# Optimization experiments

Measured on AMD Instinct MI355X. Metric: run time of the kernel, lower is better.

The kernel has to match this reference:

```python
import jax, jax.numpy as jnp
import numpy as np

N = 8192          # num atoms
APM = 32          # atoms per molecule
M = N // APM      # 256 molecules
FEAT = 100        # hidden_channels == num_filters
NG = 25           # num gaussians
K = 28            # knn neighbors
L = 4             # num interaction blocks
CUTOFF = 6.0
LOG2 = float(np.log(2.0))


def ssp(x):
    # pyg ShiftedSoftplus: softplus(x) - log(2)
    return jax.nn.softplus(x) - LOG2


def setup_inputs() -> dict:
    key = jax.random.key(0)
    ks = jax.random.split(key, 16)
    z = jax.random.randint(ks[0], (N,), 1, 100)
    pos = jax.random.normal(ks[1], (N, 3), jnp.float32) * 2.0
    ptr = jnp.arange(0, N + APM, APM)  # [M+1] molecule boundaries

    def w(k, shape, fan):
        return (jax.random.normal(k, shape, jnp.float32) / np.sqrt(fan)).astype(jnp.float32)

    def b(k, shape):
        return jax.random.normal(k, shape, jnp.float32) * 0.01

    kb = jax.random.split(ks[15], 8)
    H = FEAT // 2
    return {
        "z": z,
        "pos": pos,
        "ptr": ptr,
        "emb": jax.random.normal(ks[2], (100, FEAT), jnp.float32),
        "mlp_w1": w(ks[3], (L, NG, FEAT), NG),
        "mlp_b1": b(kb[0], (L, FEAT)),
        "mlp_w2": w(ks[4], (L, FEAT, FEAT), FEAT),
        "mlp_b2": b(kb[1], (L, FEAT)),
        "lin1_w": w(ks[5], (L, FEAT, FEAT), FEAT),
        "lin2_w": w(ks[6], (L, FEAT, FEAT), FEAT),
        "lin2_b": b(kb[2], (L, FEAT)),
        "lin_w": w(ks[7], (L, FEAT, FEAT), FEAT),
        "lin_b": b(kb[3], (L, FEAT)),
        "out_w1": w(ks[8], (FEAT, H), FEAT),
        "out_b1": b(kb[4], (H,)),
        "out_w2": w(ks[9], (H, 1), H),
        "out_b2": b(kb[5], (1,)),
    }


def reference(z, pos, ptr, emb, mlp_w1, mlp_b1, mlp_w2, mlp_b2,
              lin1_w, lin2_w, lin2_b, lin_w, lin_b,
              out_w1, out_b1, out_w2, out_b2):
    n = z.shape[0]
    m = ptr.shape[0] - 1

    # ptr -> per-atom batch ids (index_fill + cumsum; OOB index N dropped)
    flag = jnp.zeros((n,), jnp.int32).at[ptr].set(1, mode="drop")
    flag = flag.at[0].set(0)
    batch = jnp.cumsum(flag)

    # ---- KNN interaction graph (full NxN pairwise distances + masking + topk)
    diff = pos[:, None, :] - pos[None, :, :]           # [N,N,3]
    d2 = jnp.sum(diff * diff, axis=-1)                  # [N,N]
    ar = jnp.arange(n)
    mask = (ar[:, None] == ar[None, :]) \
         | (batch[:, None] != batch[None, :]) \
         | (d2 > CUTOFF * CUTOFF)
    dist = jnp.where(mask, CUTOFF, jnp.sqrt(jnp.where(mask, 1.0, d2)))
    neg, idx = jax.lax.top_k(-dist, K)                  # k nearest per row
    ew = -neg.reshape(-1)                               # edge distances [N*K]
    src = idx.reshape(-1)                               # source atoms j; target of edge (i,m) is i

    # ---- Gaussian smearing
    offset = jnp.linspace(0.0, CUTOFF, NG)
    coeff = -0.5 / (offset[1] - offset[0]) ** 2
    ea = jnp.exp(coeff * (ew[:, None] - offset[None, :]) ** 2)  # [E,NG]

    # cosine cutoff (zero weight for padded edges at dist==cutoff)
    ccut = 0.5 * (jnp.cos(ew * jnp.pi / CUTOFF) + 1.0)          # [E]

    h = emb[z]                                                   # [N,F]
    f = h.shape[1]
    for l in range(L):
        # filter network on edge attributes
        Wf = ssp(ea @ mlp_w1[l] + mlp_b1[l]) @ mlp_w2[l] + mlp_b2[l]
        Wf = Wf * ccut[:, None]                                  # [E,F]
        # CFConv: lin1 -> gather*filter -> sum over k neighbors -> lin2
        x1 = h @ lin1_w[l]                                       # [N,F]
        msg = x1[src] * Wf                                       # [E,F]
        agg = msg.reshape(n, K, f).sum(axis=1)                   # each node i has exactly K incoming edges
        v = ssp(agg @ lin2_w[l] + lin2_b[l]) @ lin_w[l] + lin_b[l]
        h = h + v

    # readout head
    h = ssp(h @ out_w1 + out_b1)
    per_atom = (h @ out_w2 + out_b2).reshape(-1)                 # [N]
    return jax.ops.segment_sum(per_atom, batch, num_segments=m) # per-molecule energy [M]
```

## Files before the change

### kernel.cpp

```cpp
#include <hip/hip_runtime.h>
#include <math.h>

#define APM   32
#define NMOL  256
#define FEAT  100
#define NPAD  112
#define LAYERS 4
#define NTHREADS 1024
#define NWAVES   16
#define G_TBL 1024
#define TSTR  128
#define X1STR 132

typedef _Float16 f16x8 __attribute__((ext_vector_type(8)));
typedef _Float16 f16x2 __attribute__((ext_vector_type(2)));
typedef float    f32x4 __attribute__((ext_vector_type(4)));
typedef float    f32x2 __attribute__((ext_vector_type(2)));

#define L1F_OFF 0
#define L2F_OFF 14336
#define LVF_OFF 28672
#define LWTOT   43008
#define WTOTAL  (4*LWTOT)

#define PREP_BLOCKS 672
#define TBL_BLOCKS  128

__device__ __forceinline__ float sspf(float x){
  return __logf(1.0f + __expf(x)) - 0.69314718056f;
}

__global__ __launch_bounds__(256) void prep_all(
    const float* __restrict__ lin1_w, const float* __restrict__ lin2_w,
    const float* __restrict__ lin_w,
    const float* __restrict__ mlp_w1, const float* __restrict__ mlp_b1,
    const float* __restrict__ mlp_w2, const float* __restrict__ mlp_b2,
    _Float16* __restrict__ outw, float* __restrict__ tbl)
{
  if (blockIdx.x < PREP_BLOCKS){
    int gid = blockIdx.x*256 + threadIdx.x;
    int l = gid / LWTOT;
    int r = gid - l*LWTOT;
    const float* W; int e;
    if (r < 14336)      { W = lin1_w + l*10000; e = r; }
    else if (r < 28672) { W = lin2_w + l*10000; e = r - 14336; }
    else                { W = lin_w  + l*10000; e = r - 28672; }
    int j = e & 7, L = (e >> 3) & 63, tile = e >> 9;
    int kc = tile / 7, nt = tile - kc*7;
    int k = kc*32 + ((L >> 4) << 3) + j;
    int f = nt*16 + (L & 15);
    float v = (k < 100 && f < FEAT) ? W[k*FEAT + f] : 0.0f;
    outw[gid] = (_Float16)v;
    return;
  }
  __shared__ float sW2[10000];
  __shared__ float sW1[2500];
  __shared__ float sB1[100], sB2[100];
  __shared__ float sT[4][100];
  int bid = blockIdx.x - PREP_BLOCKS;
  int l = bid >> 5;
  int s0 = (bid & 31) * 32;
  int tid = threadIdx.x, wv = tid >> 6, lane = tid & 63;
  for (int i = tid; i < 10000; i += 256) sW2[i] = mlp_w2[l*10000 + i];
  for (int i = tid; i < 2500;  i += 256) sW1[i] = mlp_w1[l*2500 + i];
  if (tid < 100) sB1[tid] = mlp_b1[l*100 + tid];
  if (tid >= 128 && tid < 228) sB2[tid-128] = mlp_b2[l*100 + tid-128];
  __syncthreads();
  #pragma unroll 1
  for (int si = 0; si < 8; si++){
    int s = s0 + wv*8 + si;
    float d = 6.0f * (float)s / (float)(G_TBL - 1);
    float ea[25];
    #pragma unroll
    for (int g = 0; g < 25; g++){
      float u = d - 0.25f*(float)g;
      ea[g] = __expf(-8.0f*u*u);
    }
    #pragma unroll
    for (int kk = 0; kk < 2; kk++){
      int k = lane + kk*64;
      if (k < 100){
        float acc = sB1[k];
        #pragma unroll
        for (int g = 0; g < 25; g++)
          acc += ea[g] * sW1[g*100 + k];
        sT[wv][k] = sspf(acc);
      }
    }
    float cc = 0.5f*(__cosf(d*0.52359877559f) + 1.0f);
    #pragma unroll
    for (int ff = 0; ff < 2; ff++){
      int f = lane + ff*64;
      float o = 0.0f;
      if (f < 100){
        o = sB2[f];
        for (int k = 0; k < 100; k++)
          o += sT[wv][k] * sW2[k*100 + f];
        o *= cc;
      }
      tbl[((size_t)l*G_TBL + s)*TSTR + f] = o;
    }
  }
}

__device__ __forceinline__ void cpw(_Float16* dst, const _Float16* src, int n16){
  const uint4* s = (const uint4*)src;
  uint4* d = (uint4*)dst;
  for (int i = threadIdx.x; i < n16; i += NTHREADS) d[i] = s[i];
}

__global__ __launch_bounds__(1024)
__attribute__((amdgpu_waves_per_eu(4, 4)))
void schnet_mega(
    const int* __restrict__ z, const float* __restrict__ pos,
    const float* __restrict__ emb, const _Float16* __restrict__ wf,
    const float* __restrict__ tbl,
    const float* __restrict__ lin2_b, const float* __restrict__ lin_b,
    const float* __restrict__ out_w1, const float* __restrict__ out_b1,
    const float* __restrict__ out_w2, const float* __restrict__ out_b2,
    float* __restrict__ out)
{
  __shared__ __align__(16) _Float16 sWA[43008];
  __shared__ __align__(16) _Float16 sAf[APM*136];
  __shared__ __align__(16) _Float16 sBf[APM*136];
  __shared__ __align__(16) float    sX1[APM*X1STR];
  __shared__ __align__(16) float    sH [APM*NPAD];
  __shared__ float sD [APM*33];
  __shared__ float sB2l[NPAD], sBlv[NPAD];
  __shared__ float sPos[APM*3];
  __shared__ float sPart[NWAVES];

  int tid = threadIdx.x, lane = tid & 63, wv = tid >> 6;
  int q = lane >> 4, n = lane & 15;
  int mol = blockIdx.x, mb = mol*APM;

  if (tid < 96) sPos[tid] = pos[mb*3 + tid];
  if (tid < 512){
    int r0 = tid >> 4, c0 = 112 + (tid & 15);
    sBf[r0*136 + c0] = (_Float16)0.0f;
  }
  if (tid >= 512 && tid < 512 + APM*20){
    int i = tid - 512;
    int r = i/20, c = 112 + (i - r*20);
    sX1[r*X1STR + c] = 0.0f;
  }
  for (int i = tid; i < APM*136; i += NTHREADS){
    int r = i/136, c = i - r*136;
    float v = (c < FEAT) ? emb[z[mb+r]*FEAT + c] : 0.0f;
    sAf[i] = (_Float16)v;
    if (c < NPAD) sH[r*NPAD + c] = v;
  }
  __syncthreads();
  for (int p = tid; p < APM*APM; p += NTHREADS){
    int i = p >> 5, j = p & 31;
    float dx = sPos[i*3+0]-sPos[j*3+0];
    float dy = sPos[i*3+1]-sPos[j*3+1];
    float dz = sPos[i*3+2]-sPos[j*3+2];
    float d2 = dx*dx + dy*dy + dz*dz;
    sD[i*33+j] = (d2 > 36.0f) ? 6.0f : sqrtf(d2);
  }
  __syncthreads();
  if (tid < APM){
    float dd[32];
    #pragma unroll
    for (int j = 0; j < 32; j++) dd[j] = sD[tid*33+j];
    dd[tid] = 1e30f;
    unsigned dropped = 0u;
    for (int rr = 0; rr < 4; rr++){
      float mx = -1.0f; int mj = 0;
      #pragma unroll
      for (int j = 0; j < 32; j++){
        bool ok = !((dropped>>j)&1u) && (dd[j] > mx);
        mx = ok ? dd[j] : mx;  mj = ok ? j : mj;
      }
      dropped |= 1u << mj;
    }
    #pragma unroll
    for (int j = 0; j < 32; j++)
      if ((dropped>>j)&1u) sD[tid*33+j] = 6.0f;
  }
  __syncthreads();

  for (int l = 0; l < LAYERS; l++){
    const _Float16* wl = wf + l*LWTOT;
    const float* tb = tbl + (size_t)l*G_TBL*TSTR;
    cpw(sWA, wl + L1F_OFF, 14336/8);
    if (tid < 224){
      int w = tid/112, i = tid - w*112;
      float v = (i < FEAT) ? (w==0 ? lin2_b : lin_b)[l*FEAT + i] : 0.0f;
      (w==0 ? sB2l : sBlv)[i] = v;
    }
    __syncthreads();
    for (int tau = wv; tau < 14; tau += NWAVES){
      int mt = tau/7, nt = tau - mt*7;
      f32x4 acc = {0.0f,0.0f,0.0f,0.0f};
      #pragma unroll
      for (int kc = 0; kc < 4; kc++){
        f16x8 a = *(const f16x8*)&sAf[(mt*16+n)*136 + kc*32 + q*8];
        f16x8 b = *(const f16x8*)&sWA[((kc*7+nt)*64 + lane)*8];
        acc = __builtin_amdgcn_mfma_f32_16x16x32_f16(a, b, acc, 0, 0, 0);
      }
      #pragma unroll
      for (int r = 0; r < 4; r++)
        sX1[(mt*16+q*4+r)*X1STR + nt*16+n] = acc[r];
    }
    __syncthreads();
    cpw(sWA + 14336, wl + L2F_OFF, 28672/8);
    {
      int fb = 2*lane;
      const float* rpb = tb + fb;
      #pragma unroll 1
      for (int t = 0; t < 2; t++){
        int a = wv*2 + t;
        if (lane < 56){
          f32x2 agg = {0.0f, 0.0f};
          #pragma unroll 1
          for (int j0 = 0; j0 < 32; j0 += 4){
            float frv[4]; f32x2 w0[4], w1[4];
            #pragma unroll
            for (int u = 0; u < 4; u++){
              float d = sD[a*33 + j0 + u];
              float un = d * (float)((G_TBL-1)/6.0);
              int s = (int)un;
              s = (s > G_TBL-2) ? (G_TBL-2) : s;
              frv[u] = un - (float)s;
              const float* rp = rpb + s*TSTR;
              w0[u] = *(const f32x2*)rp;
              w1[u] = *(const f32x2*)(rp + TSTR);
            }
            #pragma unroll
            for (int u = 0; u < 4; u++){
              f32x2 w = w0[u] + frv[u]*(w1[u] - w0[u]);
              f32x2 x = *(const f32x2*)&sX1[(j0+u)*X1STR + fb];
              agg += w * x;
            }
          }
          *(f16x2*)&sAf[a*136 + fb] =
              (f16x2){(_Float16)agg.x, (_Float16)agg.y};
        } else {
          *(f16x2*)&sAf[a*136 + fb] = (f16x2){(_Float16)0.0f, (_Float16)0.0f};
        }
      }
    }
    __syncthreads();
    for (int tau = wv; tau < 14; tau += NWAVES){
      int mt = tau/7, nt = tau - mt*7;
      f32x4 acc = {0.0f,0.0f,0.0f,0.0f};
      #pragma unroll
      for (int kc = 0; kc < 4; kc++){
        f16x8 a = *(const f16x8*)&sAf[(mt*16+n)*136 + kc*32 + q*8];
        f16x8 b = *(const f16x8*)&sWA[14336 + ((kc*7+nt)*64 + lane)*8];
        acc = __builtin_amdgcn_mfma_f32_16x16x32_f16(a, b, acc, 0, 0, 0);
      }
      float bb = sB2l[nt*16+n];
      #pragma unroll
      for (int r = 0; r < 4; r++)
        sBf[(mt*16+q*4+r)*136 + nt*16+n] = (_Float16)sspf(acc[r] + bb);
    }
    __syncthreads();
    for (int tau = wv; tau < 14; tau += NWAVES){
      int mt = tau/7, nt = tau - mt*7;
      f32x4 acc = {0.0f,0.0f,0.0f,0.0f};
      #pragma unroll
      for (int kc = 0; kc < 4; kc++){
        f16x8 a = *(const f16x8*)&sBf[(mt*16+n)*136 + kc*32 + q*8];
        f16x8 b = *(const f16x8*)&sWA[28672 + ((kc*7+nt)*64 + lane)*8];
        acc = __builtin_amdgcn_mfma_f32_16x16x32_f16(a, b, acc, 0, 0, 0);
      }
      int f = nt*16 + n;
      if (f < FEAT){
        float bb = sBlv[f];
        #pragma unroll
        for (int r = 0; r < 4; r++){
          int row = mt*16 + q*4 + r;
          float hn = sH[row*NPAD + f] + acc[r] + bb;
          sH[row*NPAD + f] = hn;
          sAf[row*136 + f] = (_Float16)hn;
        }
      }
    }
    __syncthreads();
  }

  float* rw = (float*)sWA;
  for (int i = tid; i < 5000; i += NTHREADS) rw[i] = out_w1[i];
  if (tid < 50){ sB2l[tid] = out_b1[tid]; sBlv[tid] = out_w2[tid]; }
  __syncthreads();
  float ob2 = out_b2[0];
  float partial = 0.0f;
  for (int t = 0; t < 2; t++){
    int a = wv*2 + t;
    float u = 0.0f;
    if (lane < 50){
      u = sB2l[lane];
      #pragma unroll 4
      for (int c = 0; c < FEAT; c++)
        u += sH[a*NPAD + c] * rw[c*50 + lane];
      u = sspf(u) * sBlv[lane];
    }
    #pragma unroll
    for (int s = 1; s < 64; s <<= 1) u += __shfl_xor(u, s);
    partial += u + ob2;
  }
  if (lane == 0) sPart[wv] = partial;
  __syncthreads();
  if (tid == 0){
    float s = 0.0f;
    #pragma unroll
    for (int i = 0; i < NWAVES; i++) s += sPart[i];
    out[mol] = s;
  }
}

extern "C" void kernel_launch(void* const* d_in, const int* in_sizes, int n_in,
                              void* d_out, int out_size, void* d_ws, size_t ws_size,
                              hipStream_t stream)
{
  const int*   z      = (const int*)  d_in[0];
  const float* pos    = (const float*)d_in[1];
  const float* emb    = (const float*)d_in[3];
  const float* mlp_w1 = (const float*)d_in[4];
  const float* mlp_b1 = (const float*)d_in[5];
  const float* mlp_w2 = (const float*)d_in[6];
  const float* mlp_b2 = (const float*)d_in[7];
  const float* lin1_w = (const float*)d_in[8];
  const float* lin2_w = (const float*)d_in[9];
  const float* lin2_b = (const float*)d_in[10];
  const float* lin_w  = (const float*)d_in[11];
  const float* lin_b  = (const float*)d_in[12];
  const float* out_w1 = (const float*)d_in[13];
  const float* out_b1 = (const float*)d_in[14];
  const float* out_w2 = (const float*)d_in[15];
  const float* out_b2 = (const float*)d_in[16];

  _Float16* wfrag = (_Float16*)d_ws;
  float*    tbl   = (float*)((char*)d_ws + WTOTAL*2);

  prep_all<<<PREP_BLOCKS + TBL_BLOCKS, 256, 0, stream>>>(
      lin1_w, lin2_w, lin_w, mlp_w1, mlp_b1, mlp_w2, mlp_b2, wfrag, tbl);
  schnet_mega<<<NMOL, NTHREADS, 0, stream>>>(z, pos, emb, wfrag, tbl,
      lin2_b, lin_b, out_w1, out_b1, out_w2, out_b2, (float*)d_out);
}
```

Baseline: 201.4 us.

## Prefetch next layer's lin1 weights during last GEMM and split aggregation across half-waves

Moves the copy of the next layer's lin1 weights and biases to the end of the previous layer, overlapping it with the final GEMM, and removes one barrier per layer by double-buffering the bias arrays. The table-interpolation aggregation is restructured so that each half-wave handles one atom in a single pass, with each lane covering four strided features instead of two adjacent ones. This removes the idle lanes and the serial two-atom loop. Global table reads become scalar rather than float2, and the strided addresses may change how well they coalesce.

```diff
diff --git a/kernel.cpp b/kernel.cpp
--- a/kernel.cpp
+++ b/kernel.cpp
@@ -13,9 +13,7 @@
 #define X1STR 132
 
 typedef _Float16 f16x8 __attribute__((ext_vector_type(8)));
-typedef _Float16 f16x2 __attribute__((ext_vector_type(2)));
 typedef float    f32x4 __attribute__((ext_vector_type(4)));
-typedef float    f32x2 __attribute__((ext_vector_type(2)));
 
 #define L1F_OFF 0
 #define L2F_OFF 14336
@@ -126,7 +124,7 @@
   __shared__ __align__(16) float    sX1[APM*X1STR];
   __shared__ __align__(16) float    sH [APM*NPAD];
   __shared__ float sD [APM*33];
-  __shared__ float sB2l[NPAD], sBlv[NPAD];
+  __shared__ float sB2l[2][NPAD], sBlv[2][NPAD];
   __shared__ float sPos[APM*3];
   __shared__ float sPart[NWAVES];
 
@@ -139,8 +137,7 @@
     int r0 = tid >> 4, c0 = 112 + (tid & 15);
     sBf[r0*136 + c0] = (_Float16)0.0f;
   }
-  if (tid >= 512 && tid < 512 + APM*20){
-    int i = tid - 512;
+  for (int i = tid; i < APM*20; i += NTHREADS){
     int r = i/20, c = 112 + (i - r*20);
     sX1[r*X1STR + c] = 0.0f;
   }
@@ -149,6 +146,12 @@
     float v = (c < FEAT) ? emb[z[mb+r]*FEAT + c] : 0.0f;
     sAf[i] = (_Float16)v;
     if (c < NPAD) sH[r*NPAD + c] = v;
+  }
+  cpw(sWA, wf + L1F_OFF, 14336/8);
+  if (tid < 224){
+    int w = tid/112, i = tid - w*112;
+    float v = (i < FEAT) ? (w==0 ? lin2_b : lin_b)[i] : 0.0f;
+    (w==0 ? sB2l[0] : sBlv[0])[i] = v;
   }
   __syncthreads();
   for (int p = tid; p < APM*APM; p += NTHREADS){
@@ -184,11 +187,62 @@
   for (int l = 0; l < LAYERS; l++){
     const _Float16* wl = wf + l*LWTOT;
     const float* tb = tbl + (size_t)l*G_TBL*TSTR;
-    cpw(sWA, wl + L1F_OFF, 14336/8);
-    if (tid < 224){
-      int w = tid/112, i = tid - w*112;
-      float v = (i < FEAT) ? (w==0 ? lin2_b : lin_b)[l*FEAT + i] : 0.0f;
-      (w==0 ? sB2l : sBlv)[i] = v;
+    int cur = l & 1;
+    for (int tau = wv; tau < 14; tau += NWAVES){
+      int mt = tau/7, nt = tau - mt*7;
+      f32x4 acc = {0.0f,0.0f,0.0f,0.0f};
+      #pragma unroll
+      for (int kc = 0; kc < 4; kc++){
+        f16x8 a = *(const f16x8*)&sAf[(mt*16+n)*136 + kc*32 + q*8];
+        f16x8 b = *(const f16x8*)&sWA[((kc*7+nt)*64 + lane)*8];
+        acc = __builtin_amdgcn_mfma_f32_16x16x32_f16(a, b, acc, 0, 0, 0);
+      }
+      #pragma unroll
+      for (int r = 0; r < 4; r++)
+        sX1[(mt*16+q*4+r)*X1STR + nt*16+n] = acc[r];
+    }
+    __syncthreads();
+    cpw(sWA + 14336, wl + L2F_OFF, 28672/8);
+    {
+      int half = lane >> 5, L = lane & 31;
+      int a = wv*2 + half;
+      int arow = a*33;
+      float agg0=0.0f, agg1=0.0f, agg2=0.0f, agg3=0.0f;
+      #pragma unroll 1
+      for (int j0 = 0; j0 < 32; j0 += 4){
+        int off[4]; float frv[4];
+        #pragma unroll
+        for (int u = 0; u < 4; u++){
+          float d = sD[arow + j0 + u];
+          float un = d * (float)((G_TBL-1)/6.0);
+          int s = (int)un;
+          s = (s > G_TBL-2) ? (G_TBL-2) : s;
+          frv[u] = un - (float)s;
+          off[u] = s*TSTR + L;
+        }
+        float w0[4][4], w1[4][4];
+        #pragma unroll
+        for (int u = 0; u < 4; u++){
+          #pragma unroll
+          for (int c = 0; c < 4; c++){
+            w0[u][c] = tb[off[u] + c*32];
+            w1[u][c] = tb[off[u] + TSTR + c*32];
+          }
+        }
+        #pragma unroll
+        for (int u = 0; u < 4; u++){
+          int xb = (j0+u)*X1STR + L;
+          agg0 += (w0[u][0] + frv[u]*(w1[u][0]-w0[u][0])) * sX1[xb];
+          agg1 += (w0[u][1] + frv[u]*(w1[u][1]-w0[u][1])) * sX1[xb+32];
+          agg2 += (w0[u][2] + frv[u]*(w1[u][2]-w0[u][2])) * sX1[xb+64];
+          agg3 += (w0[u][3] + frv[u]*(w1[u][3]-w0[u][3])) * sX1[xb+96];
+        }
+      }
+      int ab = a*136 + L;
+      sAf[ab]    = (_Float16)agg0;
+      sAf[ab+32] = (_Float16)agg1;
+      sAf[ab+64] = (_Float16)agg2;
+      sAf[ab+96] = (_Float16)agg3;
     }
     __syncthreads();
     for (int tau = wv; tau < 14; tau += NWAVES){
@@ -197,50 +251,13 @@
       #pragma unroll
       for (int kc = 0; kc < 4; kc++){
         f16x8 a = *(const f16x8*)&sAf[(mt*16+n)*136 + kc*32 + q*8];
-        f16x8 b = *(const f16x8*)&sWA[((kc*7+nt)*64 + lane)*8];
+        f16x8 b = *(const f16x8*)&sWA[14336 + ((kc*7+nt)*64 + lane)*8];
         acc = __builtin_amdgcn_mfma_f32_16x16x32_f16(a, b, acc, 0, 0, 0);
       }
+      float bb = sB2l[cur][nt*16+n];
       #pragma unroll
       for (int r = 0; r < 4; r++)
-        sX1[(mt*16+q*4+r)*X1STR + nt*16+n] = acc[r];
-    }
-    __syncthreads();
-    cpw(sWA + 14336, wl + L2F_OFF, 28672/8);
-    {
-      int fb = 2*lane;
-      const float* rpb = tb + fb;
-      #pragma unroll 1
-      for (int t = 0; t < 2; t++){
-        int a = wv*2 + t;
-        if (lane < 56){
-          f32x2 agg = {0.0f, 0.0f};
-          #pragma unroll 1
-          for (int j0 = 0; j0 < 32; j0 += 4){
-            float frv[4]; f32x2 w0[4], w1[4];
-            #pragma unroll
-            for (int u = 0; u < 4; u++){
-              float d = sD[a*33 + j0 + u];
-              float un = d * (float)((G_TBL-1)/6.0);
-              int s = (int)un;
-              s = (s > G_TBL-2) ? (G_TBL-2) : s;
-              frv[u] = un - (float)s;
-              const float* rp = rpb + s*TSTR;
-              w0[u] = *(const f32x2*)rp;
-              w1[u] = *(const f32x2*)(rp + TSTR);
-            }
-            #pragma unroll
-            for (int u = 0; u < 4; u++){
-              f32x2 w = w0[u] + frv[u]*(w1[u] - w0[u]);
-              f32x2 x = *(const f32x2*)&sX1[(j0+u)*X1STR + fb];
-              agg += w * x;
-            }
-          }
-          *(f16x2*)&sAf[a*136 + fb] =
-              (f16x2){(_Float16)agg.x, (_Float16)agg.y};
-        } else {
-          *(f16x2*)&sAf[a*136 + fb] = (f16x2){(_Float16)0.0f, (_Float16)0.0f};
-        }
-      }
+        sBf[(mt*16+q*4+r)*136 + nt*16+n] = (_Float16)sspf(acc[r] + bb);
     }
     __syncthreads();
     for (int tau = wv; tau < 14; tau += NWAVES){
@@ -248,28 +265,13 @@
       f32x4 acc = {0.0f,0.0f,0.0f,0.0f};
       #pragma unroll
       for (int kc = 0; kc < 4; kc++){
-        f16x8 a = *(const f16x8*)&sAf[(mt*16+n)*136 + kc*32 + q*8];
-        f16x8 b = *(const f16x8*)&sWA[14336 + ((kc*7+nt)*64 + lane)*8];
-        acc = __builtin_amdgcn_mfma_f32_16x16x32_f16(a, b, acc, 0, 0, 0);
-      }
-      float bb = sB2l[nt*16+n];
-      #pragma unroll
-      for (int r = 0; r < 4; r++)
-        sBf[(mt*16+q*4+r)*136 + nt*16+n] = (_Float16)sspf(acc[r] + bb);
-    }
-    __syncthreads();
-    for (int tau = wv; tau < 14; tau += NWAVES){
-      int mt = tau/7, nt = tau - mt*7;
-      f32x4 acc = {0.0f,0.0f,0.0f,0.0f};
-      #pragma unroll
-      for (int kc = 0; kc < 4; kc++){
         f16x8 a = *(const f16x8*)&sBf[(mt*16+n)*136 + kc*32 + q*8];
         f16x8 b = *(const f16x8*)&sWA[28672 + ((kc*7+nt)*64 + lane)*8];
         acc = __builtin_amdgcn_mfma_f32_16x16x32_f16(a, b, acc, 0, 0, 0);
       }
       int f = nt*16 + n;
       if (f < FEAT){
-        float bb = sBlv[f];
+        float bb = sBlv[cur][f];
         #pragma unroll
         for (int r = 0; r < 4; r++){
           int row = mt*16 + q*4 + r;
@@ -279,12 +281,20 @@
         }
       }
     }
+    if (l < LAYERS-1){
+      cpw(sWA, wl + LWTOT + L1F_OFF, 14336/8);
+      if (tid < 224){
+        int w = tid/112, i = tid - w*112;
+        float v = (i < FEAT) ? (w==0 ? lin2_b : lin_b)[(l+1)*FEAT + i] : 0.0f;
+        (w==0 ? sB2l[cur^1] : sBlv[cur^1])[i] = v;
+      }
+    }
     __syncthreads();
   }
 
   float* rw = (float*)sWA;
   for (int i = tid; i < 5000; i += NTHREADS) rw[i] = out_w1[i];
-  if (tid < 50){ sB2l[tid] = out_b1[tid]; sBlv[tid] = out_w2[tid]; }
+  if (tid < 50){ sB2l[0][tid] = out_b1[tid]; sBlv[0][tid] = out_w2[tid]; }
   __syncthreads();
   float ob2 = out_b2[0];
   float partial = 0.0f;
@@ -292,11 +302,11 @@
     int a = wv*2 + t;
     float u = 0.0f;
     if (lane < 50){
-      u = sB2l[lane];
+      u = sB2l[0][lane];
       #pragma unroll 4
       for (int c = 0; c < FEAT; c++)
         u += sH[a*NPAD + c] * rw[c*50 + lane];
-      u = sspf(u) * sBlv[lane];
+      u = sspf(u) * sBlv[0][lane];
     }
     #pragma unroll
     for (int s = 1; s < 64; s <<= 1) u += __shfl_xor(u, s);
```

Measured after the change: 174.8 us. 13.2% less time.

## Read MFMA weights directly from global, precompute table offsets, pipeline filter gathers

Applied to the files above, without the earlier changes.

Drops the 86 KB shared-memory staging buffer for the layer weights. MFMA B-operands, biases and readout weights now load straight from global memory, which removes the copy loops and barriers and shrinks LDS use. Per-pair table offsets and interpolation fractions are computed once before the layer loop instead of in every layer. The filter-aggregation loop is rewritten so each half-wave handles one atom with 4 features per lane and double-buffered software-pipelined gathers. The risk is that repeated global or L2 loads of the weights replace cheap LDS reads.

```diff
diff --git a/kernel.cpp b/kernel.cpp
--- a/kernel.cpp
+++ b/kernel.cpp
@@ -13,9 +13,7 @@
 #define X1STR 132
 
 typedef _Float16 f16x8 __attribute__((ext_vector_type(8)));
-typedef _Float16 f16x2 __attribute__((ext_vector_type(2)));
 typedef float    f32x4 __attribute__((ext_vector_type(4)));
-typedef float    f32x2 __attribute__((ext_vector_type(2)));
 
 #define L1F_OFF 0
 #define L2F_OFF 14336
@@ -103,12 +101,6 @@
   }
 }
 
-__device__ __forceinline__ void cpw(_Float16* dst, const _Float16* src, int n16){
-  const uint4* s = (const uint4*)src;
-  uint4* d = (uint4*)dst;
-  for (int i = threadIdx.x; i < n16; i += NTHREADS) d[i] = s[i];
-}
-
 __global__ __launch_bounds__(1024)
 __attribute__((amdgpu_waves_per_eu(4, 4)))
 void schnet_mega(
@@ -120,14 +112,14 @@
     const float* __restrict__ out_w2, const float* __restrict__ out_b2,
     float* __restrict__ out)
 {
-  __shared__ __align__(16) _Float16 sWA[43008];
   __shared__ __align__(16) _Float16 sAf[APM*136];
   __shared__ __align__(16) _Float16 sBf[APM*136];
   __shared__ __align__(16) float    sX1[APM*X1STR];
   __shared__ __align__(16) float    sH [APM*NPAD];
-  __shared__ float sD [APM*33];
-  __shared__ float sB2l[NPAD], sBlv[NPAD];
-  __shared__ float sPos[APM*3];
+  __shared__ float sD  [APM*33];
+  __shared__ int   sOff[APM*33];
+  __shared__ float sFr [APM*33];
+  __shared__ float sPos[96];
   __shared__ float sPart[NWAVES];
 
   int tid = threadIdx.x, lane = tid & 63, wv = tid >> 6;
@@ -139,8 +131,7 @@
     int r0 = tid >> 4, c0 = 112 + (tid & 15);
     sBf[r0*136 + c0] = (_Float16)0.0f;
   }
-  if (tid >= 512 && tid < 512 + APM*20){
-    int i = tid - 512;
+  for (int i = tid; i < APM*20; i += NTHREADS){
     int r = i/20, c = 112 + (i - r*20);
     sX1[r*X1STR + c] = 0.0f;
   }
@@ -176,19 +167,77 @@
       dropped |= 1u << mj;
     }
     #pragma unroll
-    for (int j = 0; j < 32; j++)
-      if ((dropped>>j)&1u) sD[tid*33+j] = 6.0f;
+    for (int j = 0; j < 32; j++){
+      float d = ((dropped>>j)&1u) ? 6.0f : dd[j];
+      float un = d * (float)((G_TBL-1)/6.0);
+      int s = (int)un;
+      s = (s > G_TBL-2) ? (G_TBL-2) : s;
+      sOff[tid*33+j] = s*TSTR;
+      sFr [tid*33+j] = un - (float)s;
+    }
   }
   __syncthreads();
 
   for (int l = 0; l < LAYERS; l++){
-    const _Float16* wl = wf + l*LWTOT;
+    const _Float16* w1b = wf + l*LWTOT + L1F_OFF;
+    const _Float16* w2b = wf + l*LWTOT + L2F_OFF;
+    const _Float16* wvb = wf + l*LWTOT + LVF_OFF;
     const float* tb = tbl + (size_t)l*G_TBL*TSTR;
-    cpw(sWA, wl + L1F_OFF, 14336/8);
-    if (tid < 224){
-      int w = tid/112, i = tid - w*112;
-      float v = (i < FEAT) ? (w==0 ? lin2_b : lin_b)[l*FEAT + i] : 0.0f;
-      (w==0 ? sB2l : sBlv)[i] = v;
+    for (int tau = wv; tau < 14; tau += NWAVES){
+      int mt = tau/7, nt = tau - mt*7;
+      f32x4 acc = {0.0f,0.0f,0.0f,0.0f};
+      #pragma unroll
+      for (int kc = 0; kc < 4; kc++){
+        f16x8 av = *(const f16x8*)&sAf[(mt*16+n)*136 + kc*32 + q*8];
+        f16x8 bv = *(const f16x8*)&w1b[((kc*7+nt)*64 + lane)*8];
+        acc = __builtin_amdgcn_mfma_f32_16x16x32_f16(av, bv, acc, 0, 0, 0);
+      }
+      #pragma unroll
+      for (int r = 0; r < 4; r++)
+        sX1[(mt*16+q*4+r)*X1STR + nt*16+n] = acc[r];
+    }
+    __syncthreads();
+    {
+      int half = lane >> 5, L = lane & 31;
+      int a = wv*2 + half, arow = a*33;
+      float ag0=0.0f, ag1=0.0f, ag2=0.0f, ag3=0.0f;
+      f32x4 A0[4], A1[4]; float fA[4];
+      f32x4 B0[4], B1[4]; float fB[4];
+
+#define GLD(J0, V0, V1, FR)                                            \
+      { _Pragma("unroll")                                              \
+        for (int u = 0; u < 4; u++){                                   \
+          const float* r0 = tb + (sOff[arow + (J0) + u] + L);          \
+          FR[u] = sFr[arow + (J0) + u];                                \
+          V0[u][0] = r0[0];       V0[u][1] = r0[32];                   \
+          V0[u][2] = r0[64];      V0[u][3] = r0[96];                   \
+          V1[u][0] = r0[TSTR];    V1[u][1] = r0[TSTR+32];              \
+          V1[u][2] = r0[TSTR+64]; V1[u][3] = r0[TSTR+96];              \
+        } }
+#define GCMP(J0, V0, V1, FR)                                           \
+      { _Pragma("unroll")                                              \
+        for (int u = 0; u < 4; u++){                                   \
+          const float* xp = &sX1[((J0)+u)*X1STR + L];                  \
+          f32x4 wl_ = V0[u] + FR[u]*(V1[u] - V0[u]);                   \
+          ag0 += wl_[0]*xp[0];  ag1 += wl_[1]*xp[32];                  \
+          ag2 += wl_[2]*xp[64]; ag3 += wl_[3]*xp[96];                  \
+        } }
+
+      GLD(0, A0, A1, fA)
+      #pragma unroll
+      for (int b = 0; b < 8; b += 2){
+        GLD((b+1)*4, B0, B1, fB)
+        GCMP(b*4, A0, A1, fA)
+        if (b+2 < 8) GLD((b+2)*4, A0, A1, fA)
+        GCMP((b+1)*4, B0, B1, fB)
+      }
+#undef GLD
+#undef GCMP
+      int ab = a*136 + L;
+      sAf[ab]    = (_Float16)ag0;
+      sAf[ab+32] = (_Float16)ag1;
+      sAf[ab+64] = (_Float16)ag2;
+      sAf[ab+96] = (_Float16)ag3;
     }
     __syncthreads();
     for (int tau = wv; tau < 14; tau += NWAVES){
@@ -196,51 +245,15 @@
       f32x4 acc = {0.0f,0.0f,0.0f,0.0f};
       #pragma unroll
       for (int kc = 0; kc < 4; kc++){
-        f16x8 a = *(const f16x8*)&sAf[(mt*16+n)*136 + kc*32 + q*8];
-        f16x8 b = *(const f16x8*)&sWA[((kc*7+nt)*64 + lane)*8];
-        acc = __builtin_amdgcn_mfma_f32_16x16x32_f16(a, b, acc, 0, 0, 0);
-      }
+        f16x8 av = *(const f16x8*)&sAf[(mt*16+n)*136 + kc*32 + q*8];
+        f16x8 bv = *(const f16x8*)&w2b[((kc*7+nt)*64 + lane)*8];
+        acc = __builtin_amdgcn_mfma_f32_16x16x32_f16(av, bv, acc, 0, 0, 0);
+      }
+      int f = nt*16 + n;
+      float bb = (f < FEAT) ? lin2_b[l*FEAT + f] : 0.0f;
       #pragma unroll
       for (int r = 0; r < 4; r++)
-        sX1[(mt*16+q*4+r)*X1STR + nt*16+n] = acc[r];
-    }
-    __syncthreads();
-    cpw(sWA + 14336, wl + L2F_OFF, 28672/8);
-    {
-      int fb = 2*lane;
-      const float* rpb = tb + fb;
-      #pragma unroll 1
-      for (int t = 0; t < 2; t++){
-        int a = wv*2 + t;
-        if (lane < 56){
-          f32x2 agg = {0.0f, 0.0f};
-          #pragma unroll 1
-          for (int j0 = 0; j0 < 32; j0 += 4){
-            float frv[4]; f32x2 w0[4], w1[4];
-            #pragma unroll
-            for (int u = 0; u < 4; u++){
-              float d = sD[a*33 + j0 + u];
-              float un = d * (float)((G_TBL-1)/6.0);
-              int s = (int)un;
-              s = (s > G_TBL-2) ? (G_TBL-2) : s;
-              frv[u] = un - (float)s;
-              const float* rp = rpb + s*TSTR;
-              w0[u] = *(const f32x2*)rp;
-              w1[u] = *(const f32x2*)(rp + TSTR);
-            }
-            #pragma unroll
-            for (int u = 0; u < 4; u++){
-              f32x2 w = w0[u] + frv[u]*(w1[u] - w0[u]);
-              f32x2 x = *(const f32x2*)&sX1[(j0+u)*X1STR + fb];
-              agg += w * x;
-            }
-          }
-          *(f16x2*)&sAf[a*136 + fb] =
-              (f16x2){(_Float16)agg.x, (_Float16)agg.y};
-        } else {
-          *(f16x2*)&sAf[a*136 + fb] = (f16x2){(_Float16)0.0f, (_Float16)0.0f};
-        }
-      }
+        sBf[(mt*16+q*4+r)*136 + f] = (_Float16)sspf(acc[r] + bb);
     }
     __syncthreads();
     for (int tau = wv; tau < 14; tau += NWAVES){
@@ -248,28 +261,13 @@
       f32x4 acc = {0.0f,0.0f,0.0f,0.0f};
       #pragma unroll
       for (int kc = 0; kc < 4; kc++){
-        f16x8 a = *(const f16x8*)&sAf[(mt*16+n)*136 + kc*32 + q*8];
-        f16x8 b = *(const f16x8*)&sWA[14336 + ((kc*7+nt)*64 + lane)*8];
-        acc = __builtin_amdgcn_mfma_f32_16x16x32_f16(a, b, acc, 0, 0, 0);
-      }
-      float bb = sB2l[nt*16+n];
-      #pragma unroll
-      for (int r = 0; r < 4; r++)
-        sBf[(mt*16+q*4+r)*136 + nt*16+n] = (_Float16)sspf(acc[r] + bb);
-    }
-    __syncthreads();
-    for (int tau = wv; tau < 14; tau += NWAVES){
-      int mt = tau/7, nt = tau - mt*7;
-      f32x4 acc = {0.0f,0.0f,0.0f,0.0f};
-      #pragma unroll
-      for (int kc = 0; kc < 4; kc++){
-        f16x8 a = *(const f16x8*)&sBf[(mt*16+n)*136 + kc*32 + q*8];
-        f16x8 b = *(const f16x8*)&sWA[28672 + ((kc*7+nt)*64 + lane)*8];
-        acc = __builtin_amdgcn_mfma_f32_16x16x32_f16(a, b, acc, 0, 0, 0);
+        f16x8 av = *(const f16x8*)&sBf[(mt*16+n)*136 + kc*32 + q*8];
+        f16x8 bv = *(const f16x8*)&wvb[((kc*7+nt)*64 + lane)*8];
+        acc = __builtin_amdgcn_mfma_f32_16x16x32_f16(av, bv, acc, 0, 0, 0);
       }
       int f = nt*16 + n;
       if (f < FEAT){
-        float bb = sBlv[f];
+        float bb = lin_b[l*FEAT + f];
         #pragma unroll
         for (int r = 0; r < 4; r++){
           int row = mt*16 + q*4 + r;
@@ -282,21 +280,17 @@
     __syncthreads();
   }
 
-  float* rw = (float*)sWA;
-  for (int i = tid; i < 5000; i += NTHREADS) rw[i] = out_w1[i];
-  if (tid < 50){ sB2l[tid] = out_b1[tid]; sBlv[tid] = out_w2[tid]; }
-  __syncthreads();
   float ob2 = out_b2[0];
   float partial = 0.0f;
   for (int t = 0; t < 2; t++){
     int a = wv*2 + t;
     float u = 0.0f;
     if (lane < 50){
-      u = sB2l[lane];
+      u = out_b1[lane];
       #pragma unroll 4
       for (int c = 0; c < FEAT; c++)
-        u += sH[a*NPAD + c] * rw[c*50 + lane];
-      u = sspf(u) * sBlv[lane];
+        u += sH[a*NPAD + c] * out_w1[c*50 + lane];
+      u = sspf(u) * out_w2[lane];
     }
     #pragma unroll
     for (int s = 1; s < 64; s <<= 1) u += __shfl_xor(u, s);
```

Measured after the change: 180.9 us. -10.2%, faster.
